# Optimization experiments

Hardware: AMD Instinct MI355X
Metric: run time of the kernel (lower is better)

Reference implementation:

```python
import jax, jax.numpy as jnp
import numpy as np

# Scaled Llama backbone (NF4 dequant-matmul == dense matmul math) + LoRA(q,v) + cls head
L, V, D, H, F, R, C = 4, 32000, 2048, 16, 8192, 16, 3
HD = D // H  # 128, matches real Llama head_dim
ALPHA_OVER_R = 32.0 / R
EPS = 1e-5
NEG = -1e9


def setup_inputs() -> dict:
    B, S = 2, 1024
    keys = iter(jax.random.split(jax.random.key(0), 40))

    def rn(shape, s=0.02):
        return jax.random.normal(next(keys), shape, dtype=jnp.float32) * s

    return {
        "input_ids": jax.random.randint(next(keys), (B, S), 0, V),
        "attention_mask": jnp.ones((B, S), dtype=jnp.int32),
        "embed": rn((V, D)),
        "Wq": rn((L, D, D)), "Wk": rn((L, D, D)), "Wv": rn((L, D, D)), "Wo": rn((L, D, D)),
        "Aq": rn((L, R, D)), "Bq": rn((L, D, R)), "Av": rn((L, R, D)), "Bv": rn((L, D, R)),
        "Wg": rn((L, F, D)), "Wu": rn((L, F, D)), "Wd": rn((L, D, F)),
        "norm1": jnp.ones((L, D)), "norm2": jnp.ones((L, D)), "final_norm": jnp.ones((D,)),
        "head_W1": rn((D, D)), "head_b1": jnp.zeros((D,)),
        "head_W2": rn((C, D)), "head_b2": jnp.zeros((C,)),
    }


def _rms(x, w):
    return x * w * jax.lax.rsqrt(jnp.mean(x * x, -1, keepdims=True) + EPS)


def _rope_tables(S):
    inv = 1.0 / (10000.0 ** (jnp.arange(0, HD, 2, dtype=jnp.float32) / HD))
    f = jnp.outer(jnp.arange(S, dtype=jnp.float32), inv)  # [S, HD//2]
    emb = jnp.concatenate([f, f], -1)                      # [S, HD]
    return jnp.cos(emb), jnp.sin(emb)


def _rot(x):
    return jnp.concatenate([-x[..., HD // 2:], x[..., :HD // 2]], -1)


def reference(input_ids, attention_mask, embed, Wq, Wk, Wv, Wo, Aq, Bq, Av, Bv,
              Wg, Wu, Wd, norm1, norm2, final_norm, head_W1, head_b1, head_W2, head_b2):
    B, S = input_ids.shape
    x = embed[input_ids]                                   # [B,S,D]
    cos, sin = _rope_tables(S)
    causal = jnp.tril(jnp.ones((S, S), dtype=bool))
    mask = jnp.where(causal[None, None], 0.0, NEG) \
        + (1.0 - attention_mask.astype(jnp.float32))[:, None, None, :] * NEG  # [B,1,S,S]

    for l in range(L):  # small fixed layer count
        h = _rms(x, norm1[l])

        def proj(W):
            return jnp.einsum('bsd,ed->bse', h, W)

        def lora(A, Bm):
            return ALPHA_OVER_R * jnp.einsum('bsr,er->bse', jnp.einsum('bsd,rd->bsr', h, A), Bm)

        q = (proj(Wq[l]) + lora(Aq[l], Bq[l])).reshape(B, S, H, HD)
        k = proj(Wk[l]).reshape(B, S, H, HD)
        v = (proj(Wv[l]) + lora(Av[l], Bv[l])).reshape(B, S, H, HD)
        q = q * cos[None, :, None, :] + _rot(q) * sin[None, :, None, :]
        k = k * cos[None, :, None, :] + _rot(k) * sin[None, :, None, :]

        scores = jnp.einsum('bqhd,bkhd->bhqk', q, k) / np.float32(np.sqrt(HD)) + mask
        attn = jax.nn.softmax(scores, -1)
        o = jnp.einsum('bhqk,bkhd->bqhd', attn, v).reshape(B, S, D)
        x = x + jnp.einsum('bsd,ed->bse', o, Wo[l])

        h2 = _rms(x, norm2[l])
        g = jnp.einsum('bsd,fd->bsf', h2, Wg[l])
        u = jnp.einsum('bsd,fd->bsf', h2, Wu[l])
        x = x + jnp.einsum('bsf,df->bsd', jax.nn.silu(g) * u, Wd[l])

    x = _rms(x, final_norm)
    # LlamaForSequenceClassification pooling at last non-pad token; score = Identity
    idx = jnp.sum(attention_mask, -1) - 1
    pooled = x[jnp.arange(B), idx].astype(jnp.float32)     # [B, D]
    # head_layer (dropout = identity in eval)
    h = jnp.tanh(pooled @ head_W1.T + head_b1)
    return h @ head_W2.T + head_b2                          # [B, C]
```

## Files before the change

kernel.cpp:

```cpp
#include <hip/hip_runtime.h>

#define NLAYER 4
#define DMODEL 2048
#define NHEAD  16
#define HEADD  128
#define FFDIM  8192
#define RLORA  16
#define SEQLEN 1024
#define NBATCH 2
#define NTOK   (NBATCH*SEQLEN)
#define QKVS   6144

typedef __bf16 bf16x8 __attribute__((ext_vector_type(8)));
typedef float  f32x4  __attribute__((ext_vector_type(4)));
typedef unsigned short us8 __attribute__((ext_vector_type(8)));

__device__ __forceinline__ unsigned short f2b(float f) {
  unsigned int u = __builtin_bit_cast(unsigned int, f);
  u += 0x7FFFu + ((u >> 16) & 1u);
  return (unsigned short)(u >> 16);
}
__device__ __forceinline__ float b2f(unsigned short s) {
  unsigned int u = ((unsigned int)s) << 16;
  return __builtin_bit_cast(float, u);
}
__device__ __forceinline__ int vswz(int d) {
  return (((d >> 2) & 7) ^ ((d & 3) << 1)) << 4;
}
typedef __attribute__((address_space(1))) const void* gas_t;
typedef __attribute__((address_space(3))) void* las_t;
__device__ __forceinline__ void gload16(const void* g, void* l) {
  __builtin_amdgcn_global_load_lds((gas_t)g, (las_t)l, 16, 0, 0);
}

__global__ void k_embed(const int* __restrict__ ids, const float* __restrict__ emb,
                        float* __restrict__ x) {
  int row = blockIdx.x;
  int id = ids[row];
  const float4* src = (const float4*)(emb + (size_t)id * DMODEL);
  float4* dst = (float4*)(x + (size_t)row * DMODEL);
  for (int i = threadIdx.x; i < DMODEL / 4; i += 256) dst[i] = src[i];
}

__global__ void k_cvt16(const float* __restrict__ s, unsigned short* __restrict__ d, int n8) {
  int stride = gridDim.x * 256;
  for (int i = blockIdx.x * 256 + threadIdx.x; i < n8; i += stride) {
    size_t si = (size_t)i * 2;
    float4 a = ((const float4*)s)[si];
    float4 b = ((const float4*)s)[si + 1];
    us8 o;
    o[0]=f2b(a.x); o[1]=f2b(a.y); o[2]=f2b(a.z); o[3]=f2b(a.w);
    o[4]=f2b(b.x); o[5]=f2b(b.y); o[6]=f2b(b.z); o[7]=f2b(b.w);
    ((us8*)d)[i] = o;
  }
}

__global__ void k_cvtqkv(const float* __restrict__ Wq, const float* __restrict__ Wk,
                         const float* __restrict__ Wv, unsigned short* __restrict__ d) {
  const size_t DD8 = (size_t)DMODEL * DMODEL / 8;
  const int n8 = (int)(NLAYER * 3 * DD8);
  int stride = gridDim.x * 256;
  for (int i = blockIdx.x * 256 + threadIdx.x; i < n8; i += stride) {
    int blk = i >> 19;
    int lay = blk / 3;
    int ten = blk - lay * 3;
    int off = i & ((1 << 19) - 1);
    const float* s = (ten == 0 ? Wq : ten == 1 ? Wk : Wv) + (size_t)lay * DMODEL * DMODEL;
    float4 a = ((const float4*)s)[(size_t)off * 2];
    float4 b = ((const float4*)s)[(size_t)off * 2 + 1];
    us8 o;
    o[0]=f2b(a.x); o[1]=f2b(a.y); o[2]=f2b(a.z); o[3]=f2b(a.w);
    o[4]=f2b(b.x); o[5]=f2b(b.y); o[6]=f2b(b.z); o[7]=f2b(b.w);
    ((us8*)(d))[(size_t)i] = o;
  }
}

__global__ void k_rmsnorm(const float* __restrict__ x, const float* __restrict__ w,
                          unsigned short* __restrict__ h) {
  int row = blockIdx.x, t = threadIdx.x;
  const float* xr = x + (size_t)row * DMODEL;
  float4 a = ((const float4*)xr)[t];
  float4 b = ((const float4*)xr)[t + 256];
  float ss = a.x*a.x + a.y*a.y + a.z*a.z + a.w*a.w
           + b.x*b.x + b.y*b.y + b.z*b.z + b.w*b.w;
  for (int m = 32; m; m >>= 1) ss += __shfl_xor(ss, m);
  __shared__ float red[4];
  if ((t & 63) == 0) red[t >> 6] = ss;
  __syncthreads();
  ss = red[0] + red[1] + red[2] + red[3];
  float rs = rsqrtf(ss * (1.0f / DMODEL) + 1e-5f);
  float4 wa = ((const float4*)w)[t];
  float4 wb = ((const float4*)w)[t + 256];
  ushort4 oa, ob;
  oa.x = f2b(a.x * wa.x * rs); oa.y = f2b(a.y * wa.y * rs);
  oa.z = f2b(a.z * wa.z * rs); oa.w = f2b(a.w * wa.w * rs);
  ob.x = f2b(b.x * wb.x * rs); ob.y = f2b(b.y * wb.y * rs);
  ob.z = f2b(b.z * wb.z * rs); ob.w = f2b(b.w * wb.w * rs);
  ushort4* hr = (ushort4*)(h + (size_t)row * DMODEL);
  hr[t] = oa;
  hr[t + 256] = ob;
}

__global__ __launch_bounds__(512, 4)
void k_ffn(const unsigned short* __restrict__ A, const unsigned short* __restrict__ Bgw,
           const unsigned short* __restrict__ Buw, unsigned short* __restrict__ act,
           int N, int K, int ldc) {
  __shared__ unsigned short As[8192];
  __shared__ unsigned short Gs[8192];
  __shared__ unsigned short Us[8192];
  const int t = threadIdx.x, l = t & 63, w = t >> 6;
  const int wm = w >> 2, wn = w & 3;
  const int nbx = gridDim.x;
  const int nmt = gridDim.y;
  const int nwg = nbx * nmt;
  const int bid = blockIdx.y * nbx + blockIdx.x;
  const int sid = (bid & 7) * (nwg >> 3) + (bid >> 3);
  const int m0 = (sid % nmt) << 7;
  const int n0 = (sid / nmt) << 7;
  const int srow = (w << 3) + (l >> 3);
  const int gcol = 8 * ((l & 7) ^ ((srow >> 1) & 7));
  const unsigned short* Ap = A   + (size_t)(m0 + srow) * K + gcol;
  const unsigned short* Gp = Bgw + (size_t)(n0 + srow) * K + gcol;
  const unsigned short* Up = Buw + (size_t)(n0 + srow) * K + gcol;
  const size_t r64K = (size_t)64 * K;
  unsigned short* AsW = As + (w << 9);
  unsigned short* GsW = Gs + (w << 9);
  unsigned short* UsW = Us + (w << 9);
  const int cl = l & 15, lh = l >> 4;
  const int fR = (cl >> 1) & 7;
  f32x4 ag[4][2], au[4][2];
  #pragma unroll
  for (int mi = 0; mi < 4; mi++)
    #pragma unroll
    for (int ni = 0; ni < 2; ni++) {
      f32x4 z = {0.f,0.f,0.f,0.f};
      ag[mi][ni] = z; au[mi][ni] = z;
    }

  for (int kt = 0; kt < K; kt += 64) {
    gload16(Ap + kt,          AsW);
    gload16(Ap + kt + r64K,   AsW + 4096);
    gload16(Gp + kt,          GsW);
    gload16(Gp + kt + r64K,   GsW + 4096);
    gload16(Up + kt,          UsW);
    gload16(Up + kt + r64K,   UsW + 4096);
    __syncthreads();
    #pragma unroll
    for (int kh = 0; kh < 2; kh++) {
      const int so = ((kh * 4 + lh) ^ fR) << 4;
      bf16x8 af[4], bg[2], bu[2];
      #pragma unroll
      for (int mi = 0; mi < 4; mi++)
        af[mi] = *(const bf16x8*)((const char*)As + (wm*64 + mi*16 + cl) * 128 + so);
      #pragma unroll
      for (int ni = 0; ni < 2; ni++) {
        bg[ni] = *(const bf16x8*)((const char*)Gs + (wn*32 + ni*16 + cl) * 128 + so);
        bu[ni] = *(const bf16x8*)((const char*)Us + (wn*32 + ni*16 + cl) * 128 + so);
      }
      #pragma unroll
      for (int mi = 0; mi < 4; mi++)
        #pragma unroll
        for (int ni = 0; ni < 2; ni++) {
          ag[mi][ni] = __builtin_amdgcn_mfma_f32_16x16x32_bf16(af[mi], bg[ni], ag[mi][ni], 0, 0, 0);
          au[mi][ni] = __builtin_amdgcn_mfma_f32_16x16x32_bf16(af[mi], bu[ni], au[mi][ni], 0, 0, 0);
        }
    }
    __syncthreads();
  }
  const int rbase = lh << 2;
  #pragma unroll
  for (int mi = 0; mi < 4; mi++) {
    #pragma unroll
    for (int ni = 0; ni < 2; ni++) {
      #pragma unroll
      for (int rr = 0; rr < 4; rr++) {
        int row = m0 + wm * 64 + mi * 16 + rbase + rr;
        int col = n0 + wn * 32 + ni * 16 + cl;
        float gv = ag[mi][ni][rr];
        float uv = au[mi][ni][rr];
        float val = gv / (1.0f + __expf(-gv)) * uv;
        act[(size_t)row * ldc + col] = f2b(val);
      }
    }
  }
}

template<int MODE>
__global__ __launch_bounds__(256, 4)
void k_gemm6(const unsigned short* __restrict__ A, const unsigned short* __restrict__ B,
             float* __restrict__ Cf, unsigned short* __restrict__ Cb,
             const float* __restrict__ Res, const unsigned short* __restrict__ Gaux,
             int N, int K, int ldc) {
  __shared__ unsigned short As[4096];
  __shared__ unsigned short Bs[8192];
  const int t = threadIdx.x, l = t & 63, w = t >> 6;
  const int nbx = gridDim.x;
  const int nmt = gridDim.y;
  const int bid = blockIdx.y * nbx + blockIdx.x;
  const int xcd = bid & 7;
  const int local = bid >> 3;
  const int cm = nmt >> 2;
  const int cn = nbx >> 1;
  const int m0 = ((xcd & 3) * cm + (local % cm)) << 6;
  const int n0 = ((xcd >> 2) * cn + (local / cm)) << 7;
  const int srow = (w << 3) + (l >> 3);
  const int gcol = 8 * ((l & 7) ^ ((srow >> 1) & 7));
  const unsigned short* Ag = A + (size_t)(m0 + srow) * K + gcol;
  const unsigned short* Bg = B + (size_t)(n0 + srow) * K + gcol;
  const size_t r32K = (size_t)32 * K;
  unsigned short* AsW = As + (w << 9);
  unsigned short* BsW = Bs + (w << 9);
  const int cl = l & 15, lh = l >> 4;
  const int fR = (cl >> 1) & 7;
  f32x4 acc[4][2];
  #pragma unroll
  for (int mi = 0; mi < 4; mi++)
    #pragma unroll
    for (int ni = 0; ni < 2; ni++) { f32x4 z = {0.f,0.f,0.f,0.f}; acc[mi][ni] = z; }

  for (int kt = 0; kt < K; kt += 64) {
    gload16(Ag + kt,          AsW);
    gload16(Ag + kt +   r32K, AsW + 2048);
    gload16(Bg + kt,          BsW);
    gload16(Bg + kt +   r32K, BsW + 2048);
    gload16(Bg + kt + 2*r32K, BsW + 4096);
    gload16(Bg + kt + 3*r32K, BsW + 6144);
    __syncthreads();
    #pragma unroll
    for (int kh = 0; kh < 2; kh++) {
      const int so = ((kh * 4 + lh) ^ fR) << 4;
      bf16x8 af[4], bf[2];
      #pragma unroll
      for (int mi = 0; mi < 4; mi++)
        af[mi] = *(const bf16x8*)((const char*)As + (mi*16 + cl) * 128 + so);
      #pragma unroll
      for (int ni = 0; ni < 2; ni++)
        bf[ni] = *(const bf16x8*)((const char*)Bs + (w*32 + ni*16 + cl) * 128 + so);
      #pragma unroll
      for (int mi = 0; mi < 4; mi++)
        #pragma unroll
        for (int ni = 0; ni < 2; ni++)
          acc[mi][ni] = __builtin_amdgcn_mfma_f32_16x16x32_bf16(af[mi], bf[ni], acc[mi][ni], 0, 0, 0);
    }
    __syncthreads();
  }
  const int rbase = lh << 2;
  #pragma unroll
  for (int mi = 0; mi < 4; mi++) {
    #pragma unroll
    for (int ni = 0; ni < 2; ni++) {
      #pragma unroll
      for (int rr = 0; rr < 4; rr++) {
        int row = m0 + mi * 16 + rbase + rr;
        int col = n0 + w * 32 + ni * 16 + cl;
        size_t idx = (size_t)row * ldc + col;
        float val = acc[mi][ni][rr];
        if constexpr (MODE == 0) Cf[idx] = val;
        if constexpr (MODE == 1) Cf[idx] = val + Res[idx];
        if constexpr (MODE == 2) Cb[idx] = f2b(val);
        if constexpr (MODE == 3) {
          float gv = b2f(Gaux[idx]);
          val *= gv / (1.0f + __expf(-gv));
          Cb[idx] = f2b(val);
        }
      }
    }
  }
}

__global__ __launch_bounds__(256, 4)
void k_gemm7(const unsigned short* __restrict__ A, const unsigned short* __restrict__ B,
             float* __restrict__ Cf, int N, int K, int ldc,
             const float* __restrict__ ltq, const float* __restrict__ ltv,
             const float* __restrict__ lbq, const float* __restrict__ lbv) {
  __shared__ unsigned short As[4096];
  __shared__ unsigned short Bs[8192];
  const int t = threadIdx.x, l = t & 63, w = t >> 6;
  const int nbx = gridDim.x;
  const int nmt = gridDim.y;
  const int nwg = nbx * nmt;
  const int bid = blockIdx.y * nbx + blockIdx.x;
  const int sid = (bid & 7) * (nwg >> 3) + (bid >> 3);
  const int m0 = (sid % nmt) << 6;
  const int n0 = (sid / nmt) << 7;
  const int srow = (w << 3) + (l >> 3);
  const int gcol = 8 * ((l & 7) ^ ((srow >> 1) & 7));
  const unsigned short* Ag = A + (size_t)(m0 + srow) * K + gcol;
  const unsigned short* Bg = B + (size_t)(n0 + srow) * K + gcol;
  const size_t r32K = (size_t)32 * K;
  unsigned short* AsW = As + (w << 9);
  unsigned short* BsW = Bs + (w << 9);
  const int cl = l & 15, lh = l >> 4;
  const int fR = (cl >> 1) & 7;
  f32x4 acc[4][2];
  #pragma unroll
  for (int mi = 0; mi < 4; mi++)
    #pragma unroll
    for (int ni = 0; ni < 2; ni++) { f32x4 z = {0.f,0.f,0.f,0.f}; acc[mi][ni] = z; }

  for (int kt = 0; kt < K; kt += 64) {
    gload16(Ag + kt,          AsW);
    gload16(Ag + kt +   r32K, AsW + 2048);
    gload16(Bg + kt,          BsW);
    gload16(Bg + kt +   r32K, BsW + 2048);
    gload16(Bg + kt + 2*r32K, BsW + 4096);
    gload16(Bg + kt + 3*r32K, BsW + 6144);
    __syncthreads();
    #pragma unroll
    for (int kh = 0; kh < 2; kh++) {
      const int so = ((kh * 4 + lh) ^ fR) << 4;
      bf16x8 af[4], bf[2];
      #pragma unroll
      for (int mi = 0; mi < 4; mi++)
        af[mi] = *(const bf16x8*)((const char*)As + (mi*16 + cl) * 128 + so);
      #pragma unroll
      for (int ni = 0; ni < 2; ni++)
        bf[ni] = *(const bf16x8*)((const char*)Bs + (w*32 + ni*16 + cl) * 128 + so);
      #pragma unroll
      for (int mi = 0; mi < 4; mi++)
        #pragma unroll
        for (int ni = 0; ni < 2; ni++)
          acc[mi][ni] = __builtin_amdgcn_mfma_f32_16x16x32_bf16(af[mi], bf[ni], acc[mi][ni], 0, 0, 0);
    }
    __syncthreads();
  }
  const int rbase = lh << 2;
  #pragma unroll
  for (int ni = 0; ni < 2; ni++) {
    int col = n0 + w * 32 + ni * 16 + cl;
    const float* lt = nullptr;
    const float* lb = nullptr;
    if (col < 2048)       { lt = ltq; lb = lbq + (size_t)col * RLORA; }
    else if (col >= 4096) { lt = ltv; lb = lbv + (size_t)(col - 4096) * RLORA; }
    float4 b0 = {0,0,0,0}, b1 = b0, b2 = b0, b3 = b0;
    if (lt) {
      b0 = ((const float4*)lb)[0]; b1 = ((const float4*)lb)[1];
      b2 = ((const float4*)lb)[2]; b3 = ((const float4*)lb)[3];
    }
    #pragma unroll
    for (int mi = 0; mi < 4; mi++) {
      #pragma unroll
      for (int rr = 0; rr < 4; rr++) {
        int row = m0 + mi * 16 + rbase + rr;
        float val = acc[mi][ni][rr];
        if (lt) {
          const float4* tr = (const float4*)(lt + (size_t)row * RLORA);
          float4 t0 = tr[0], t1 = tr[1], t2 = tr[2], t3 = tr[3];
          float dt = t0.x*b0.x + t0.y*b0.y + t0.z*b0.z + t0.w*b0.w
                   + t1.x*b1.x + t1.y*b1.y + t1.z*b1.z + t1.w*b1.w
                   + t2.x*b2.x + t2.y*b2.y + t2.z*b2.z + t2.w*b2.w
                   + t3.x*b3.x + t3.y*b3.y + t3.z*b3.z + t3.w*b3.w;
          val += 2.0f * dt;
        }
        Cf[(size_t)row * ldc + col] = val;
      }
    }
  }
}

template<int MODE>
__global__ __launch_bounds__(256, 2)
void k_gemm(const unsigned short* __restrict__ A, const void* __restrict__ Bv,
            float* __restrict__ Cf, unsigned short* __restrict__ Cb,
            const float* __restrict__ Res, const unsigned short* __restrict__ Gaux,
            int N, int K, int ldc) {
  __shared__ unsigned char lds[128 * 32 * 2 * 2];
  unsigned char* As = lds;
  unsigned char* Bs = lds + 128 * 32 * 2;
  const int t = threadIdx.x;
  const int l = t & 63, w = t >> 6;
  const int wr = w >> 1, wc = w & 1;
  const int m0 = blockIdx.y << 7, n0 = blockIdx.x << 7;
  const int sr = t >> 1, skh = (t & 1) << 4;
  const int sByte = sr * 64 + (skh << 1);
  const int sSwz = (sr & 3) << 4;
  const unsigned short* Ap = A + (size_t)(m0 + sr) * K + skh;
  const float* Bp32 = (const float*)Bv + (size_t)(n0 + sr) * K + skh;
  const int kOff = (((l >> 4) << 4)) ^ ((l & 3) << 4);
  const int arow = wr * 64 + (l & 15);
  const int brow = wc * 64 + (l & 15);
  f32x4 acc[4][4];
  #pragma unroll
  for (int mi = 0; mi < 4; mi++)
    #pragma unroll
    for (int ni = 0; ni < 4; ni++) { f32x4 z = {0.f,0.f,0.f,0.f}; acc[mi][ni] = z; }

  for (int kt = 0; kt < K; kt += 32) {
    uint4 a0 = *(const uint4*)(Ap + kt);
    uint4 a1 = *(const uint4*)(Ap + kt + 8);
    *(uint4*)(As + ((sByte)      ^ sSwz)) = a0;
    *(uint4*)(As + ((sByte + 16) ^ sSwz)) = a1;
    float4 f0 = *(const float4*)(Bp32 + kt);
    float4 f1 = *(const float4*)(Bp32 + kt + 4);
    float4 f2 = *(const float4*)(Bp32 + kt + 8);
    float4 f3 = *(const float4*)(Bp32 + kt + 12);
    us8 q0, q1;
    q0[0]=f2b(f0.x); q0[1]=f2b(f0.y); q0[2]=f2b(f0.z); q0[3]=f2b(f0.w);
    q0[4]=f2b(f1.x); q0[5]=f2b(f1.y); q0[6]=f2b(f1.z); q0[7]=f2b(f1.w);
    q1[0]=f2b(f2.x); q1[1]=f2b(f2.y); q1[2]=f2b(f2.z); q1[3]=f2b(f2.w);
    q1[4]=f2b(f3.x); q1[5]=f2b(f3.y); q1[6]=f2b(f3.z); q1[7]=f2b(f3.w);
    *(us8*)(Bs + ((sByte)      ^ sSwz)) = q0;
    *(us8*)(Bs + ((sByte + 16) ^ sSwz)) = q1;
    __syncthreads();
    bf16x8 af[4], bfr[4];
    #pragma unroll
    for (int i = 0; i < 4; i++) {
      af[i]  = *(const bf16x8*)(As + (arow + 16 * i) * 64 + kOff);
      bfr[i] = *(const bf16x8*)(Bs + (brow + 16 * i) * 64 + kOff);
    }
    #pragma unroll
    for (int mi = 0; mi < 4; mi++)
      #pragma unroll
      for (int ni = 0; ni < 4; ni++)
        acc[mi][ni] = __builtin_amdgcn_mfma_f32_16x16x32_bf16(af[mi], bfr[ni], acc[mi][ni], 0, 0, 0);
    __syncthreads();
  }
  const int rbase = (l >> 4) << 2;
  const int cl = l & 15;
  #pragma unroll
  for (int mi = 0; mi < 4; mi++) {
    #pragma unroll
    for (int ni = 0; ni < 4; ni++) {
      #pragma unroll
      for (int rr = 0; rr < 4; rr++) {
        int row = m0 + wr * 64 + mi * 16 + rbase + rr;
        int col = n0 + wc * 64 + ni * 16 + cl;
        size_t idx = (size_t)row * ldc + col;
        float val = acc[mi][ni][rr];
        if constexpr (MODE == 0) Cf[idx] = val;
        if constexpr (MODE == 1) Cf[idx] = val + Res[idx];
        if constexpr (MODE == 2) Cb[idx] = f2b(val);
        if constexpr (MODE == 3) {
          float gv = b2f(Gaux[idx]);
          val *= gv / (1.0f + __expf(-gv));
          Cb[idx] = f2b(val);
        }
      }
    }
  }
}

__global__ void k_lora_down(const unsigned short* __restrict__ h, const float* __restrict__ Am,
                            float* __restrict__ tb) {
  int t = threadIdx.x;
  int m = blockIdx.x * 16 + (t >> 4), r = t & 15;
  const unsigned short* hr = h + (size_t)m * DMODEL;
  const float* ar = Am + (size_t)r * DMODEL;
  float acc = 0.f;
  for (int d = 0; d < DMODEL; d += 4) {
    ushort4 hv = *(const ushort4*)(hr + d);
    float4 av = *(const float4*)(ar + d);
    acc += b2f(hv.x)*av.x + b2f(hv.y)*av.y + b2f(hv.z)*av.z + b2f(hv.w)*av.w;
  }
  tb[(size_t)m * RLORA + r] = acc;
}

__global__ void k_lora_up(const float* __restrict__ tb, const float* __restrict__ Bm,
                          float* __restrict__ out, int ldc) {
  int tid = blockIdx.x * 256 + threadIdx.x;
  int m = tid >> 11, e = tid & (DMODEL - 1);
  const float* tr = tb + (size_t)m * RLORA;
  const float* br = Bm + (size_t)e * RLORA;
  float acc = 0.f;
  #pragma unroll
  for (int r = 0; r < RLORA; r += 4) {
    float4 tv = *(const float4*)(tr + r);
    float4 bv = *(const float4*)(br + r);
    acc += tv.x*bv.x + tv.y*bv.y + tv.z*bv.z + tv.w*bv.w;
  }
  out[(size_t)m * ldc + e] += 2.0f * acc;
}

__global__ void k_rope_table(float* __restrict__ ct, float* __restrict__ st) {
  int tid = blockIdx.x * 256 + threadIdx.x;
  int s = tid >> 6, i = tid & 63;
  float inv = __expf(-((float)i / 64.0f) * logf(10000.0f));
  float ang = (float)s * inv;
  ct[tid] = cosf(ang);
  st[tid] = sinf(ang);
}

__global__ void k_rope2(const float* __restrict__ qkv,
                        const float* __restrict__ ct, const float* __restrict__ st,
                        unsigned short* __restrict__ qb, unsigned short* __restrict__ kb,
                        unsigned short* __restrict__ vb) {
  int tid = blockIdx.x * 256 + threadIdx.x;
  int i = tid & 63;
  int hh = (tid >> 6) & (NHEAD - 1);
  int s = (tid >> 10) & (SEQLEN - 1);
  int b = tid >> 20;
  size_t ibase = ((size_t)(b * SEQLEN + s)) * QKVS + hh * HEADD;
  size_t obase = ((size_t)(b * SEQLEN + s)) * DMODEL + hh * HEADD;
  float c = ct[s * 64 + i], sn = st[s * 64 + i];
  float q0 = qkv[ibase + i], q1 = qkv[ibase + i + 64];
  qb[obase + i]      = f2b(q0 * c - q1 * sn);
  qb[obase + i + 64] = f2b(q1 * c + q0 * sn);
  float k0 = qkv[ibase + 2048 + i], k1 = qkv[ibase + 2048 + i + 64];
  kb[obase + i]      = f2b(k0 * c - k1 * sn);
  kb[obase + i + 64] = f2b(k1 * c + k0 * sn);
  vb[obase + i]      = f2b(qkv[ibase + 4096 + i]);
  vb[obase + i + 64] = f2b(qkv[ibase + 4096 + i + 64]);
}

__global__ __launch_bounds__(256, 2)
void k_attn_bf16(const unsigned short* __restrict__ qbp, const unsigned short* __restrict__ kbp,
                 const unsigned short* __restrict__ vbp, const int* __restrict__ am,
                 unsigned short* __restrict__ o, int vstride) {
  __shared__ unsigned char Kls[64 * 256];
  __shared__ unsigned char Vls[128 * 128];
  __shared__ unsigned char Pls[64 * 128];
  const int qt = blockIdx.x, hh = blockIdx.y, b = blockIdx.z;
  const int t = threadIdx.x, l = t & 63, w = t >> 6;
  const int cl = l & 15, lh = l >> 4;
  const int rbase = lh << 2;

  for (int ii = 0; ii < 4; ii++) {
    int idx = t + 256 * ii; int row = idx >> 4; int c = idx & 15;
    uint4 u = *(const uint4*)(qbp + ((size_t)(b*SEQLEN + qt*64 + row)) * DMODEL + hh * HEADD + c * 8);
    *(uint4*)(Kls + ((row * 256 + c * 16) ^ ((row & 7) << 4))) = u;
  }
  __syncthreads();
  bf16x8 qf[4];
  {
    int row = w * 16 + cl;
    int swz = (row & 7) << 4;
    #pragma unroll
    for (int kt = 0; kt < 4; kt++)
      qf[kt] = *(const bf16x8*)(Kls + ((row * 256 + kt * 64 + lh * 16) ^ swz));
  }

  f32x4 oacc[8];
  #pragma unroll
  for (int i = 0; i < 8; i++) { f32x4 z = {0.f,0.f,0.f,0.f}; oacc[i] = z; }
  float mrun[4], lrun[4];
  #pragma unroll
  for (int r = 0; r < 4; r++) { mrun[r] = -3e38f; lrun[r] = 0.f; }

  for (int kb = 0; kb <= qt; kb++) {
    __syncthreads();
    for (int ii = 0; ii < 4; ii++) {
      int idx = t + 256 * ii; int row = idx >> 4; int c = idx & 15;
      uint4 u = *(const uint4*)(kbp + ((size_t)(b*SEQLEN + kb*64 + row)) * DMODEL + hh * HEADD + c * 8);
      *(uint4*)(Kls + ((row * 256 + c * 16) ^ ((row & 7) << 4))) = u;
    }
    for (int ii = 0; ii < 4; ii++) {
      int idx = t + 256 * ii;
      int n = idx >> 4, dc = idx & 15;
      uint4 a = *(const uint4*)(vbp + ((size_t)(b*SEQLEN + kb*64 + n)) * vstride + hh * HEADD + dc * 8);
      uint4 p;
      p.x = __shfl_xor(a.x, 16); p.y = __shfl_xor(a.y, 16);
      p.z = __shfl_xor(a.z, 16); p.w = __shfl_xor(a.w, 16);
      if (!(l & 16)) {
        int d0 = dc * 8, nb = n * 2;
        unsigned int wd[8];
        wd[0] = (a.x & 0xffffu) | (p.x << 16);
        wd[1] = (a.x >> 16)     | (p.x & 0xffff0000u);
        wd[2] = (a.y & 0xffffu) | (p.y << 16);
        wd[3] = (a.y >> 16)     | (p.y & 0xffff0000u);
        wd[4] = (a.z & 0xffffu) | (p.z << 16);
        wd[5] = (a.z >> 16)     | (p.z & 0xffff0000u);
        wd[6] = (a.w & 0xffffu) | (p.w << 16);
        wd[7] = (a.w >> 16)     | (p.w & 0xffff0000u);
        #pragma unroll
        for (int e = 0; e < 8; e++)
          *(unsigned int*)(Vls + (((d0 + e) * 128 + nb) ^ vswz(d0 + e))) = wd[e];
      }
    }
    __syncthreads();
    f32x4 sacc[4];
    #pragma unroll
    for (int nt = 0; nt < 4; nt++) { f32x4 z = {0.f,0.f,0.f,0.f}; sacc[nt] = z; }
    #pragma unroll
    for (int kt = 0; kt < 4; kt++) {
      #pragma unroll
      for (int nt = 0; nt < 4; nt++) {
        int row = nt * 16 + cl;
        bf16x8 kf = *(const bf16x8*)(Kls + ((row * 256 + kt * 64 + lh * 16) ^ ((row & 7) << 4)));
        sacc[nt] = __builtin_amdgcn_mfma_f32_16x16x32_bf16(qf[kt], kf, sacc[nt], 0, 0, 0);
      }
    }
    float p[4][4];
    float mt[4] = {-3e38f, -3e38f, -3e38f, -3e38f};
    #pragma unroll
    for (int nt = 0; nt < 4; nt++) {
      int kg = kb * 64 + nt * 16 + cl;
      float pad = (1.0f - (float)am[b * SEQLEN + kg]) * (-1e9f);
      #pragma unroll
      for (int r = 0; r < 4; r++) {
        int qg = qt * 64 + w * 16 + rbase + r;
        float s = sacc[nt][r] * 0.08838834764831845f + pad;
        if (kg > qg) s = -1e30f;
        p[nt][r] = s;
        mt[r] = fmaxf(mt[r], s);
      }
    }
    #pragma unroll
    for (int r = 0; r < 4; r++) {
      float m = mt[r];
      m = fmaxf(m, __shfl_xor(m, 1)); m = fmaxf(m, __shfl_xor(m, 2));
      m = fmaxf(m, __shfl_xor(m, 4)); m = fmaxf(m, __shfl_xor(m, 8));
      mt[r] = m;
    }
    float corr[4];
    #pragma unroll
    for (int r = 0; r < 4; r++) {
      float mnew = fmaxf(mrun[r], mt[r]);
      corr[r] = __expf(mrun[r] - mnew);
      mrun[r] = mnew;
    }
    float ps[4] = {0.f, 0.f, 0.f, 0.f};
    #pragma unroll
    for (int nt = 0; nt < 4; nt++)
      #pragma unroll
      for (int r = 0; r < 4; r++) {
        p[nt][r] = __expf(p[nt][r] - mrun[r]);
        ps[r] += p[nt][r];
      }
    #pragma unroll
    for (int r = 0; r < 4; r++) {
      float s = ps[r];
      s += __shfl_xor(s, 1); s += __shfl_xor(s, 2);
      s += __shfl_xor(s, 4); s += __shfl_xor(s, 8);
      lrun[r] = lrun[r] * corr[r] + s;
    }
    #pragma unroll
    for (int nt = 0; nt < 4; nt++)
      #pragma unroll
      for (int r = 0; r < 4; r++) {
        int row = w * 16 + rbase + r;
        *(unsigned short*)(Pls + ((row * 128 + (nt * 16 + cl) * 2) ^ ((row & 7) << 4))) = f2b(p[nt][r]);
      }
    #pragma unroll
    for (int dt = 0; dt < 8; dt++)
      #pragma unroll
      for (int r = 0; r < 4; r++) oacc[dt][r] *= corr[r];
    {
      int prow = w * 16 + cl, pswz = (prow & 7) << 4;
      bf16x8 pf0 = *(const bf16x8*)(Pls + ((prow * 128 +  0 + lh * 16) ^ pswz));
      bf16x8 pf1 = *(const bf16x8*)(Pls + ((prow * 128 + 64 + lh * 16) ^ pswz));
      #pragma unroll
      for (int dt = 0; dt < 8; dt++) {
        int drow = dt * 16 + cl;
        bf16x8 vf0 = *(const bf16x8*)(Vls + ((drow * 128 +  0 + lh * 16) ^ vswz(drow)));
        bf16x8 vf1 = *(const bf16x8*)(Vls + ((drow * 128 + 64 + lh * 16) ^ vswz(drow)));
        oacc[dt] = __builtin_amdgcn_mfma_f32_16x16x32_bf16(pf0, vf0, oacc[dt], 0, 0, 0);
        oacc[dt] = __builtin_amdgcn_mfma_f32_16x16x32_bf16(pf1, vf1, oacc[dt], 0, 0, 0);
      }
    }
  }
  size_t obase = (((size_t)b * SEQLEN + qt * 64 + w * 16) * NHEAD + hh) * HEADD;
  #pragma unroll
  for (int r = 0; r < 4; r++) {
    float inv = 1.0f / lrun[r];
    int row = rbase + r;
    #pragma unroll
    for (int dt = 0; dt < 8; dt++)
      o[obase + (size_t)row * (NHEAD * HEADD) + dt * 16 + cl] = f2b(oacc[dt][r] * inv);
  }
}

__global__ void k_pool(const float* __restrict__ x, const int* __restrict__ am,
                       const float* __restrict__ fn, float* __restrict__ pooled) {
  int b = blockIdx.x, t = threadIdx.x;
  __shared__ float red[4];
  float fc = 0.f;
  for (int i = t; i < SEQLEN; i += 256) fc += (float)am[b * SEQLEN + i];
  for (int m = 32; m; m >>= 1) fc += __shfl_xor(fc, m);
  if ((t & 63) == 0) red[t >> 6] = fc;
  __syncthreads();
  int idx = (int)(red[0] + red[1] + red[2] + red[3]) - 1;
  const float* xr = x + ((size_t)b * SEQLEN + idx) * DMODEL;
  float4 a = ((const float4*)xr)[t], c = ((const float4*)xr)[t + 256];
  float ss = a.x*a.x + a.y*a.y + a.z*a.z + a.w*a.w
           + c.x*c.x + c.y*c.y + c.z*c.z + c.w*c.w;
  for (int m = 32; m; m >>= 1) ss += __shfl_xor(ss, m);
  __syncthreads();
  if ((t & 63) == 0) red[t >> 6] = ss;
  __syncthreads();
  ss = red[0] + red[1] + red[2] + red[3];
  float rs = rsqrtf(ss * (1.0f / DMODEL) + 1e-5f);
  float4 w0 = ((const float4*)fn)[t], w1 = ((const float4*)fn)[t + 256];
  float4 o0, o1;
  o0.x = a.x*rs*w0.x; o0.y = a.y*rs*w0.y; o0.z = a.z*rs*w0.z; o0.w = a.w*rs*w0.w;
  o1.x = c.x*rs*w1.x; o1.y = c.y*rs*w1.y; o1.z = c.z*rs*w1.z; o1.w = c.w*rs*w1.w;
  ((float4*)(pooled + (size_t)b * DMODEL))[t] = o0;
  ((float4*)(pooled + (size_t)b * DMODEL))[t + 256] = o1;
}

__global__ void k_head1(const float* __restrict__ pooled, const float* __restrict__ W1,
                        const float* __restrict__ b1, float* __restrict__ h1) {
  int bi = blockIdx.x;
  int b = bi >> 3, e = ((bi & 7) << 8) + threadIdx.x;
  const float* pr = pooled + (size_t)b * DMODEL;
  const float* wr = W1 + (size_t)e * DMODEL;
  float acc = 0.f;
  for (int d = 0; d < DMODEL; d += 4) {
    float4 pv = *(const float4*)(pr + d);
    float4 wv = *(const float4*)(wr + d);
    acc += pv.x*wv.x + pv.y*wv.y + pv.z*wv.z + pv.w*wv.w;
  }
  h1[(size_t)b * DMODEL + e] = tanhf(acc + b1[e]);
}

__global__ void k_head2(const float* __restrict__ h1, const float* __restrict__ W2,
                        const float* __restrict__ b2, float* __restrict__ out) {
  int bi = blockIdx.x;
  int b = bi / 3, c = bi % 3;
  int l = threadIdx.x;
  float acc = 0.f;
  for (int e = l; e < DMODEL; e += 64)
    acc += h1[(size_t)b * DMODEL + e] * W2[(size_t)c * DMODEL + e];
  for (int m = 32; m; m >>= 1) acc += __shfl_xor(acc, m);
  if (l == 0) out[b * 3 + c] = acc + b2[c];
}

__global__ void k_sentinel(float* out) {
  if (threadIdx.x < 6) out[threadIdx.x] = -12345.0f;
}

extern "C" void kernel_launch(void* const* d_in, const int* in_sizes, int n_in,
                              void* d_out, int out_size, void* d_ws, size_t ws_size,
                              hipStream_t stream) {
  const int*   ids = (const int*)d_in[0];
  const int*   am  = (const int*)d_in[1];
  const float* emb = (const float*)d_in[2];
  const float* Wq  = (const float*)d_in[3];
  const float* Wk  = (const float*)d_in[4];
  const float* Wv  = (const float*)d_in[5];
  const float* Wo  = (const float*)d_in[6];
  const float* Aq  = (const float*)d_in[7];
  const float* Bq  = (const float*)d_in[8];
  const float* Av  = (const float*)d_in[9];
  const float* Bv  = (const float*)d_in[10];
  const float* Wg  = (const float*)d_in[11];
  const float* Wu  = (const float*)d_in[12];
  const float* Wd  = (const float*)d_in[13];
  const float* n1  = (const float*)d_in[14];
  const float* n2  = (const float*)d_in[15];
  const float* fn  = (const float*)d_in[16];
  const float* hW1 = (const float*)d_in[17];
  const float* hb1 = (const float*)d_in[18];
  const float* hW2 = (const float*)d_in[19];
  const float* hb2 = (const float*)d_in[20];
  float* out = (float*)d_out;

  const size_t XOFF    = 0;
  const size_t HOFF    = 16777216;
  const size_t QBOFF   = 25165824;
  const size_t KBOFF   = 33554432;
  const size_t VBOFF   = 41943040;
  const size_t OOFF    = 50331648;
  const size_t GOFF    = 58720256;
  const size_t ACTOFF  = 92274688;
  const size_t QKV32OFF= 125829120;
  const size_t TOFF    = 176160768;
  const size_t NEED = TOFF + 131072 + 131072 + 262144 + 262144 + 16384 + 16384;
  if (ws_size < NEED) {
    k_sentinel<<<1, 64, 0, stream>>>(out);
    return;
  }
  const size_t W16OFF   = (NEED + 255) & ~(size_t)255;
  const size_t W16BYTES = 536870912ull;
  const bool   use16    = ws_size >= W16OFF + W16BYTES;

  char* ws = (char*)d_ws;
  float*          x     = (float*)(ws + XOFF);
  unsigned short* h     = (unsigned short*)(ws + HOFF);
  unsigned short* qb    = (unsigned short*)(ws + QBOFF);
  unsigned short* kb    = (unsigned short*)(ws + KBOFF);
  unsigned short* vb    = (unsigned short*)(ws + VBOFF);
  unsigned short* o     = (unsigned short*)(ws + OOFF);
  unsigned short* g     = (unsigned short*)(ws + GOFF);
  unsigned short* act   = (unsigned short*)(ws + ACTOFF);
  float*          qkv32 = (float*)(ws + QKV32OFF);
  float* tbq    = (float*)(ws + TOFF);
  float* tbv    = (float*)(ws + TOFF + 131072);
  float* ct     = (float*)(ws + TOFF + 262144);
  float* st     = (float*)(ws + TOFF + 262144 + 262144);
  float* pooled = (float*)(ws + TOFF + 262144 + 524288);
  float* h1     = (float*)(ws + TOFF + 262144 + 524288 + 16384);

  unsigned short* w16 = (unsigned short*)(ws + W16OFF);
  const size_t DD = (size_t)DMODEL * DMODEL;
  const size_t FD = (size_t)FFDIM * DMODEL;
  unsigned short* wqkv16 = w16;
  unsigned short* wo16   = w16 + 4ull * 3 * DD;
  unsigned short* wg16   = wo16 + 4ull * DD;
  unsigned short* wu16   = wg16 + 4ull * FD;
  unsigned short* wd16   = wu16 + 4ull * FD;
  if (use16) {
    k_cvtqkv<<<2048, 256, 0, stream>>>(Wq, Wk, Wv, wqkv16);
    k_cvt16<<<2048, 256, 0, stream>>>(Wo, wo16, (int)(4 * DD / 8));
    k_cvt16<<<2048, 256, 0, stream>>>(Wg, wg16, (int)(4 * FD / 8));
    k_cvt16<<<2048, 256, 0, stream>>>(Wu, wu16, (int)(4 * FD / 8));
    k_cvt16<<<2048, 256, 0, stream>>>(Wd, wd16, (int)(4 * FD / 8));
  }

  k_embed<<<NTOK, 256, 0, stream>>>(ids, emb, x);
  k_rope_table<<<SEQLEN * 64 / 256, 256, 0, stream>>>(ct, st);

  dim3 g16(16, 16), gqkv(48, 32), gffn(64, 16), gsq(16, 32), ga(SEQLEN / 64, NHEAD, NBATCH);
  for (int lay = 0; lay < NLAYER; lay++) {
    const float* Bq_l = Bq + (size_t)lay * DMODEL * RLORA;
    const float* Bv_l = Bv + (size_t)lay * DMODEL * RLORA;
    k_rmsnorm<<<NTOK, 256, 0, stream>>>(x, n1 + (size_t)lay * DMODEL, h);
    k_lora_down<<<NTOK / 16, 256, 0, stream>>>(h, Aq + (size_t)lay * RLORA * DMODEL, tbq);
    k_lora_down<<<NTOK / 16, 256, 0, stream>>>(h, Av + (size_t)lay * RLORA * DMODEL, tbv);
    if (use16) {
      k_gemm7<<<gqkv, 256, 0, stream>>>(h, wqkv16 + lay*3*DD, qkv32,
                                        QKVS, DMODEL, QKVS, tbq, tbv, Bq_l, Bv_l);
      k_rope2<<<NBATCH * SEQLEN * NHEAD * 64 / 256, 256, 0, stream>>>(qkv32, ct, st, qb, kb, vb);
      k_attn_bf16<<<ga, 256, 0, stream>>>(qb, kb, vb, am, o, DMODEL);
      k_gemm6<1><<<gsq, 256, 0, stream>>>(o, wo16 + lay*DD, x, nullptr, x, nullptr, DMODEL, DMODEL, DMODEL);
      k_rmsnorm<<<NTOK, 256, 0, stream>>>(x, n2 + (size_t)lay * DMODEL, h);
      k_ffn<<<gffn, 512, 0, stream>>>(h, wg16 + lay*FD, wu16 + lay*FD, act, FFDIM, DMODEL, FFDIM);
      k_gemm6<1><<<gsq, 256, 0, stream>>>(act, wd16 + lay*FD, x, nullptr, x, nullptr, DMODEL, FFDIM, DMODEL);
    } else {
      k_gemm<0><<<g16, 256, 0, stream>>>(h, Wq + lay*DD, qkv32,        nullptr, nullptr, nullptr, DMODEL, DMODEL, QKVS);
      k_gemm<0><<<g16, 256, 0, stream>>>(h, Wk + lay*DD, qkv32 + 2048, nullptr, nullptr, nullptr, DMODEL, DMODEL, QKVS);
      k_gemm<0><<<g16, 256, 0, stream>>>(h, Wv + lay*DD, qkv32 + 4096, nullptr, nullptr, nullptr, DMODEL, DMODEL, QKVS);
      k_lora_up<<<NTOK * DMODEL / 256, 256, 0, stream>>>(tbq, Bq_l, qkv32, QKVS);
      k_lora_up<<<NTOK * DMODEL / 256, 256, 0, stream>>>(tbv, Bv_l, qkv32 + 4096, QKVS);
      k_rope2<<<NBATCH * SEQLEN * NHEAD * 64 / 256, 256, 0, stream>>>(qkv32, ct, st, qb, kb, vb);
      k_attn_bf16<<<ga, 256, 0, stream>>>(qb, kb, vb, am, o, DMODEL);
      k_gemm<1><<<g16, 256, 0, stream>>>(o, Wo + lay*DD, x, nullptr, x, nullptr, DMODEL, DMODEL, DMODEL);
      k_rmsnorm<<<NTOK, 256, 0, stream>>>(x, n2 + (size_t)lay * DMODEL, h);
      k_gemm<2><<<dim3(64,16), 256, 0, stream>>>(h, Wg + lay*FD, nullptr, g, nullptr, nullptr, FFDIM, DMODEL, FFDIM);
      k_gemm<3><<<dim3(64,16), 256, 0, stream>>>(h, Wu + lay*FD, nullptr, act, nullptr, g, FFDIM, DMODEL, FFDIM);
      k_gemm<1><<<g16, 256, 0, stream>>>(act, Wd + lay*FD, x, nullptr, x, nullptr, DMODEL, FFDIM, DMODEL);
    }
  }
  k_pool<<<NBATCH, 256, 0, stream>>>(x, am, fn, pooled);
  k_head1<<<16, 256, 0, stream>>>(pooled, hW1, hb1, h1);
  k_head2<<<6, 64, 0, stream>>>(h1, hW2, hb2, out);
}
```

Baseline: 2.997 ms.

## Fuse RoPE and bf16 output into QKV GEMM epilogue; merge LoRA-down kernels

The QKV GEMM now remaps each wave's column tiles so that a lane holds both halves (i and i+64) of a head dimension. This lets the epilogue apply the LoRA update, the RoPE rotation and the bf16 conversion directly, writing q/k/v buffers in place of an fp32 intermediate. The separate rope kernel and the fp32 QKV round trip to global memory go away. The two LoRA-down launches are also merged into one kernel covering q and v ranks together. Together these cut launches and memory traffic, at the cost of a slightly heavier GEMM epilogue with scattered stores.

```diff
diff --git a/kernel.cpp b/kernel.cpp
--- a/kernel.cpp
+++ b/kernel.cpp
@@ -270,7 +270,10 @@
 
 __global__ __launch_bounds__(256, 4)
 void k_gemm7(const unsigned short* __restrict__ A, const unsigned short* __restrict__ B,
-             float* __restrict__ Cf, int N, int K, int ldc,
+             unsigned short* __restrict__ qb, unsigned short* __restrict__ kb,
+             unsigned short* __restrict__ vb,
+             const float* __restrict__ ct, const float* __restrict__ st,
+             int K,
              const float* __restrict__ ltq, const float* __restrict__ ltv,
              const float* __restrict__ lbq, const float* __restrict__ lbv) {
   __shared__ unsigned short As[4096];
@@ -315,7 +318,7 @@
         af[mi] = *(const bf16x8*)((const char*)As + (mi*16 + cl) * 128 + so);
       #pragma unroll
       for (int ni = 0; ni < 2; ni++)
-        bf[ni] = *(const bf16x8*)((const char*)Bs + (w*32 + ni*16 + cl) * 128 + so);
+        bf[ni] = *(const bf16x8*)((const char*)Bs + (w*16 + ni*64 + cl) * 128 + so);
       #pragma unroll
       for (int mi = 0; mi < 4; mi++)
         #pragma unroll
@@ -325,35 +328,54 @@
     __syncthreads();
   }
   const int rbase = lh << 2;
-  #pragma unroll
-  for (int ni = 0; ni < 2; ni++) {
-    int col = n0 + w * 32 + ni * 16 + cl;
-    const float* lt = nullptr;
-    const float* lb = nullptr;
-    if (col < 2048)       { lt = ltq; lb = lbq + (size_t)col * RLORA; }
-    else if (col >= 4096) { lt = ltv; lb = lbv + (size_t)(col - 4096) * RLORA; }
-    float4 b0 = {0,0,0,0}, b1 = b0, b2 = b0, b3 = b0;
-    if (lt) {
-      b0 = ((const float4*)lb)[0]; b1 = ((const float4*)lb)[1];
-      b2 = ((const float4*)lb)[2]; b3 = ((const float4*)lb)[3];
-    }
-    #pragma unroll
-    for (int mi = 0; mi < 4; mi++) {
-      #pragma unroll
-      for (int rr = 0; rr < 4; rr++) {
-        int row = m0 + mi * 16 + rbase + rr;
-        float val = acc[mi][ni][rr];
-        if (lt) {
-          const float4* tr = (const float4*)(lt + (size_t)row * RLORA);
-          float4 t0 = tr[0], t1 = tr[1], t2 = tr[2], t3 = tr[3];
-          float dt = t0.x*b0.x + t0.y*b0.y + t0.z*b0.z + t0.w*b0.w
-                   + t1.x*b1.x + t1.y*b1.y + t1.z*b1.z + t1.w*b1.w
-                   + t2.x*b2.x + t2.y*b2.y + t2.z*b2.z + t2.w*b2.w
-                   + t3.x*b3.x + t3.y*b3.y + t3.z*b3.z + t3.w*b3.w;
-          val += 2.0f * dt;
-        }
-        Cf[(size_t)row * ldc + col] = val;
-      }
+  const int i0 = (w << 4) + cl;
+  const int col_lo = n0 + i0;
+  const int reg = n0 >> 11;
+  const float* lt = nullptr;
+  const float* lb_lo = nullptr;
+  const float* lb_hi = nullptr;
+  if (reg == 0)      { lt = ltq; lb_lo = lbq + (size_t)col_lo * RLORA;
+                                 lb_hi = lbq + (size_t)(col_lo + 64) * RLORA; }
+  else if (reg == 2) { lt = ltv; lb_lo = lbv + (size_t)(col_lo - 4096) * RLORA;
+                                 lb_hi = lbv + (size_t)(col_lo - 4096 + 64) * RLORA; }
+  float4 bl0={0,0,0,0}, bl1=bl0, bl2=bl0, bl3=bl0;
+  float4 bh0=bl0, bh1=bl0, bh2=bl0, bh3=bl0;
+  if (lt) {
+    bl0 = ((const float4*)lb_lo)[0]; bl1 = ((const float4*)lb_lo)[1];
+    bl2 = ((const float4*)lb_lo)[2]; bl3 = ((const float4*)lb_lo)[3];
+    bh0 = ((const float4*)lb_hi)[0]; bh1 = ((const float4*)lb_hi)[1];
+    bh2 = ((const float4*)lb_hi)[2]; bh3 = ((const float4*)lb_hi)[3];
+  }
+  unsigned short* outp = (reg == 0 ? qb : reg == 1 ? kb : vb);
+  const int ocol = col_lo - reg * 2048;
+  #pragma unroll
+  for (int mi = 0; mi < 4; mi++) {
+    #pragma unroll
+    for (int rr = 0; rr < 4; rr++) {
+      int row = m0 + mi * 16 + rbase + rr;
+      float lo = acc[mi][0][rr];
+      float hi = acc[mi][1][rr];
+      if (lt) {
+        const float4* tr = (const float4*)(lt + (size_t)row * RLORA);
+        float4 t0 = tr[0], t1 = tr[1], t2 = tr[2], t3 = tr[3];
+        lo += 2.0f * (t0.x*bl0.x + t0.y*bl0.y + t0.z*bl0.z + t0.w*bl0.w
+                    + t1.x*bl1.x + t1.y*bl1.y + t1.z*bl1.z + t1.w*bl1.w
+                    + t2.x*bl2.x + t2.y*bl2.y + t2.z*bl2.z + t2.w*bl2.w
+                    + t3.x*bl3.x + t3.y*bl3.y + t3.z*bl3.z + t3.w*bl3.w);
+        hi += 2.0f * (t0.x*bh0.x + t0.y*bh0.y + t0.z*bh0.z + t0.w*bh0.w
+                    + t1.x*bh1.x + t1.y*bh1.y + t1.z*bh1.z + t1.w*bh1.w
+                    + t2.x*bh2.x + t2.y*bh2.y + t2.z*bh2.z + t2.w*bh2.w
+                    + t3.x*bh3.x + t3.y*bh3.y + t3.z*bh3.z + t3.w*bh3.w);
+      }
+      if (reg != 2) {
+        int s = row & (SEQLEN - 1);
+        float c = ct[s * 64 + i0], sn = st[s * 64 + i0];
+        float nlo = lo * c - hi * sn;
+        float nhi = hi * c + lo * sn;
+        lo = nlo; hi = nhi;
+      }
+      outp[(size_t)row * DMODEL + ocol]      = f2b(lo);
+      outp[(size_t)row * DMODEL + ocol + 64] = f2b(hi);
     }
   }
 }
@@ -438,6 +460,24 @@
       }
     }
   }
+}
+
+__global__ void k_lora_down2(const unsigned short* __restrict__ h,
+                             const float* __restrict__ Aq, const float* __restrict__ Av,
+                             float* __restrict__ tbq, float* __restrict__ tbv) {
+  int t = threadIdx.x;
+  int m = blockIdx.x * 8 + (t >> 5), r = t & 31;
+  const float* ar = (r < 16) ? (Aq + (size_t)r * DMODEL)
+                             : (Av + (size_t)(r - 16) * DMODEL);
+  const unsigned short* hr = h + (size_t)m * DMODEL;
+  float acc = 0.f;
+  for (int d = 0; d < DMODEL; d += 4) {
+    ushort4 hv = *(const ushort4*)(hr + d);
+    float4 av = *(const float4*)(ar + d);
+    acc += b2f(hv.x)*av.x + b2f(hv.y)*av.y + b2f(hv.z)*av.z + b2f(hv.w)*av.w;
+  }
+  if (r < 16) tbq[(size_t)m * RLORA + r] = acc;
+  else        tbv[(size_t)m * RLORA + (r - 16)] = acc;
 }
 
 __global__ void k_lora_down(const unsigned short* __restrict__ h, const float* __restrict__ Am,
@@ -804,18 +844,19 @@
     const float* Bq_l = Bq + (size_t)lay * DMODEL * RLORA;
     const float* Bv_l = Bv + (size_t)lay * DMODEL * RLORA;
     k_rmsnorm<<<NTOK, 256, 0, stream>>>(x, n1 + (size_t)lay * DMODEL, h);
-    k_lora_down<<<NTOK / 16, 256, 0, stream>>>(h, Aq + (size_t)lay * RLORA * DMODEL, tbq);
-    k_lora_down<<<NTOK / 16, 256, 0, stream>>>(h, Av + (size_t)lay * RLORA * DMODEL, tbv);
     if (use16) {
-      k_gemm7<<<gqkv, 256, 0, stream>>>(h, wqkv16 + lay*3*DD, qkv32,
-                                        QKVS, DMODEL, QKVS, tbq, tbv, Bq_l, Bv_l);
-      k_rope2<<<NBATCH * SEQLEN * NHEAD * 64 / 256, 256, 0, stream>>>(qkv32, ct, st, qb, kb, vb);
+      k_lora_down2<<<NTOK / 8, 256, 0, stream>>>(h, Aq + (size_t)lay * RLORA * DMODEL,
+                                                 Av + (size_t)lay * RLORA * DMODEL, tbq, tbv);
+      k_gemm7<<<gqkv, 256, 0, stream>>>(h, wqkv16 + lay*3*DD, qb, kb, vb, ct, st,
+                                        DMODEL, tbq, tbv, Bq_l, Bv_l);
       k_attn_bf16<<<ga, 256, 0, stream>>>(qb, kb, vb, am, o, DMODEL);
       k_gemm6<1><<<gsq, 256, 0, stream>>>(o, wo16 + lay*DD, x, nullptr, x, nullptr, DMODEL, DMODEL, DMODEL);
       k_rmsnorm<<<NTOK, 256, 0, stream>>>(x, n2 + (size_t)lay * DMODEL, h);
       k_ffn<<<gffn, 512, 0, stream>>>(h, wg16 + lay*FD, wu16 + lay*FD, act, FFDIM, DMODEL, FFDIM);
       k_gemm6<1><<<gsq, 256, 0, stream>>>(act, wd16 + lay*FD, x, nullptr, x, nullptr, DMODEL, FFDIM, DMODEL);
     } else {
+      k_lora_down<<<NTOK / 16, 256, 0, stream>>>(h, Aq + (size_t)lay * RLORA * DMODEL, tbq);
+      k_lora_down<<<NTOK / 16, 256, 0, stream>>>(h, Av + (size_t)lay * RLORA * DMODEL, tbv);
       k_gemm<0><<<g16, 256, 0, stream>>>(h, Wq + lay*DD, qkv32,        nullptr, nullptr, nullptr, DMODEL, DMODEL, QKVS);
       k_gemm<0><<<g16, 256, 0, stream>>>(h, Wk + lay*DD, qkv32 + 2048, nullptr, nullptr, nullptr, DMODEL, DMODEL, QKVS);
       k_gemm<0><<<g16, 256, 0, stream>>>(h, Wv + lay*DD, qkv32 + 4096, nullptr, nullptr, nullptr, DMODEL, DMODEL, QKVS);
```

Measured after the change: 2.628 ms. 12.3% less time.
